# Kernel tuning notes

Measured on AMD Instinct MI355X. Metric: run time of the kernel, lower is better.

Reference implementation:

```python
import jax, jax.numpy as jnp
import numpy as np

K = 8192  # num_embeddings
D = 512   # embedding_dim
BETA = 0.25


def setup_inputs() -> dict:
    key = jax.random.key(0)
    k1, k2, k3 = jax.random.split(key, 3)
    B, T = 64, 512
    latents = jax.random.normal(k1, (B, T, D), dtype=jnp.float32)
    # nn.Embedding weight initialized uniform(-1/K, 1/K)
    emb = jax.random.uniform(k2, (K, D), dtype=jnp.float32, minval=-1.0 / K, maxval=1.0 / K)
    gold_encoding_inds = jax.random.randint(k3, (B * T, 1), 0, K, dtype=jnp.int64 if jax.config.jax_enable_x64 else jnp.int32)
    return {"gold_encoding_inds": gold_encoding_inds, "latents": latents, "epc": 1, "emb": emb}


def reference(gold_encoding_inds, latents, epc, emb):
    B, T, _ = latents.shape
    flat = latents.reshape(B * T, D)  # [N, D]
    # squared euclidean distance to every codebook entry: [N, K]
    dist = (jnp.sum(flat * flat, axis=1, keepdims=True)
            + jnp.sum(emb * emb, axis=1)
            - 2.0 * jnp.matmul(flat, emb.T))
    encoding_inds = jnp.argmin(dist, axis=1)[:, None]  # [N, 1]
    # one-hot @ emb  ==  gather rows of emb
    quantized = emb[encoding_inds[:, 0]].reshape(B, T, D)
    # per-position MSE over the feature dim
    commitment_loss = jnp.mean((jax.lax.stop_gradient(quantized) - latents) ** 2, axis=-1)
    embedding_loss = jnp.mean((quantized - jax.lax.stop_gradient(latents)) ** 2, axis=-1)
    vq_loss = embedding_loss + BETA * commitment_loss  # [B, T]
    # straight-through estimator
    quantized = latents + jax.lax.stop_gradient(quantized - latents)
    correct = jnp.sum(gold_encoding_inds == encoding_inds)
    total = jnp.asarray(gold_encoding_inds.shape[0], dtype=jnp.int32)
    return quantized, vq_loss, encoding_inds.T, (correct, total)
```

## Files before the change

### kernel.cpp

```cpp
#include <hip/hip_runtime.h>
#include <math.h>

#define N_ROWS 32768
#define KCB    8192
#define DIM    512
#define BETA   0.25f
#define MARGIN 2e-3f
#define FLAG_SLACK 1e-4f
#define CAND_CAP 256

typedef __attribute__((ext_vector_type(4))) float  f32x4;

__device__ __forceinline__ unsigned short f2h(float x) {
    _Float16 h = (_Float16)x;
    return *(unsigned short*)&h;
}
__device__ __forceinline__ float h2f(unsigned short u) {
    _Float16 h = *(_Float16*)&u;
    return (float)h;
}

#define SQ_BLOCKS ((N_ROWS + KCB) / 8)
__global__ __launch_bounds__(256) void pre_kernel(
        const float* __restrict__ lat, const float* __restrict__ emb,
        float* __restrict__ row_sq, float* __restrict__ emb_sq,
        unsigned char* __restrict__ latq, unsigned char* __restrict__ embq,
        int* __restrict__ counter) {
    if (blockIdx.x < SQ_BLOCKS) {
#pragma clang fp contract(off)
        if (blockIdx.x == 0 && threadIdx.x == 0) *counter = 0;
        const int w    = threadIdx.x >> 6;
        const int lane = threadIdx.x & 63;
        const int half = lane >> 5;
        const int L    = lane & 31;
        const int b    = L >> 3, j = L & 7;
        const int row  = blockIdx.x * 8 + w * 2 + half;
        const float* p = (row < N_ROWS) ? (lat + (size_t)row * DIM)
                                        : (emb + (size_t)(row - N_ROWS) * DIM);
        const float* q = p + 128 * b + j;
        float a0 = q[0];
        float r  = a0 * a0;
        for (int i = 1; i < 16; ++i) {
            float a = q[8 * i];
            float s = a * a;
            r = r + s;
        }
        r = r + __shfl_xor(r, 1);
        r = r + __shfl_xor(r, 2);
        r = r + __shfl_xor(r, 4);
        r = r + __shfl_xor(r, 8);
        r = r + __shfl_xor(r, 16);
        if (L == 0) {
            if (row < N_ROWS) row_sq[row] = r;
            else              emb_sq[row - N_ROWS] = r;
        }
    } else {
        const size_t NL8 = (size_t)N_ROWS * DIM / 8;
        const size_t NE8 = (size_t)KCB * DIM / 8;
        size_t g = (size_t)(blockIdx.x - SQ_BLOCKS) * 256 + threadIdx.x;
        const float* src; unsigned char* dst; size_t i; float sc;
        if (g < NL8)            { src = lat; dst = latq; i = g;       sc = 1.0f; }
        else if (g < NL8 + NE8) { src = emb; dst = embq; i = g - NL8; sc = 8192.0f; }
        else return;
        float4 v0 = ((const float4*)src)[2 * i];
        float4 v1 = ((const float4*)src)[2 * i + 1];
        int lo = __builtin_amdgcn_cvt_pk_fp8_f32(v0.x * sc, v0.y * sc, 0,  false);
        lo     = __builtin_amdgcn_cvt_pk_fp8_f32(v0.z * sc, v0.w * sc, lo, true);
        int hi = __builtin_amdgcn_cvt_pk_fp8_f32(v1.x * sc, v1.y * sc, 0,  false);
        hi     = __builtin_amdgcn_cvt_pk_fp8_f32(v1.z * sc, v1.w * sc, hi, true);
        ((int2*)dst)[i] = make_int2(lo, hi);
    }
}

__device__ __forceinline__ void load16_to_lds(const void* g, void* l) {
    __builtin_amdgcn_global_load_lds(
        (const __attribute__((address_space(1))) unsigned int*)g,
        (__attribute__((address_space(3))) unsigned int*)l, 16, 0, 0);
}

__global__ __launch_bounds__(256, 3) void gemm_kernel(
        const unsigned char* __restrict__ latq,
        const unsigned char* __restrict__ embq,
        const float* __restrict__ emb_sq,
        unsigned int* __restrict__ packed) {
    __shared__ unsigned char Ac[4 * 128 * 16];
    __shared__ unsigned char Br[4 * 128 * 16];

    const int tid   = threadIdx.x;
    const int w     = tid >> 6;
    const int lane  = tid & 63;
    const int q     = lane >> 4;
    const int m16   = lane & 15;
    const int row0  = blockIdx.x * 128;
    const int code0 = blockIdx.y * 128;
    const int wc    = 64 * (w >> 1);
    const int rbase = 64 * (w & 1);

    float sev[4][4];
#pragma unroll
    for (int r = 0; r < 4; ++r)
#pragma unroll
        for (int reg = 0; reg < 4; ++reg)
            sev[r][reg] = emb_sq[code0 + wc + 16 * r + 4 * q + reg];

    f32x4 acc[4][4];
#pragma unroll
    for (int r = 0; r < 4; ++r)
#pragma unroll
        for (int c = 0; c < 4; ++c) acc[r][c] = (f32x4){0.f, 0.f, 0.f, 0.f};

    for (int k0 = 0; k0 < DIM; k0 += 64) {
#pragma unroll
        for (int i = 0; i < 4; ++i) {
            int cid = w * 4 + i;
            if (cid < 8) {
                int p = cid >> 1, h = cid & 1;
                const unsigned char* g = embq +
                    (size_t)(code0 + h * 64 + lane) * DIM + k0 + p * 16;
                load16_to_lds(g, &Ac[(p * 128 + h * 64) * 16]);
            } else {
                int c2 = cid - 8, p = c2 >> 1, h = c2 & 1;
                const unsigned char* g = latq +
                    (size_t)(row0 + h * 64 + lane) * DIM + k0 + p * 16;
                load16_to_lds(g, &Br[(p * 128 + h * 64) * 16]);
            }
        }
        __syncthreads();
#pragma unroll
        for (int kk = 0; kk < 2; ++kk) {
            long a[4], b[4];
            const int p  = 2 * kk + (q >> 1);
            const int hf = (q & 1) * 8;
#pragma unroll
            for (int r = 0; r < 4; ++r)
                a[r] = *(const long*)&Ac[(p * 128 + wc + 16 * r + m16) * 16 + hf];
#pragma unroll
            for (int c = 0; c < 4; ++c)
                b[c] = *(const long*)&Br[(p * 128 + rbase + 16 * c + m16) * 16 + hf];
#pragma unroll
            for (int r = 0; r < 4; ++r)
#pragma unroll
                for (int c = 0; c < 4; ++c)
                    acc[r][c] = __builtin_amdgcn_mfma_f32_16x16x32_fp8_fp8(
                        a[r], b[c], acc[r][c], 0, 0, 0);
        }
        __syncthreads();
    }

    const float inv = 1.0f / 4096.0f;
#pragma unroll
    for (int c = 0; c < 4; ++c) {
        unsigned pk[4];
#pragma unroll
        for (int r = 0; r < 4; ++r) {
            float s0 = sev[r][0] - acc[r][c][0] * inv;
            float s1 = sev[r][1] - acc[r][c][1] * inv;
            float s2 = sev[r][2] - acc[r][c][2] * inv;
            float s3 = sev[r][3] - acc[r][c][3] * inv;
            float mn = fminf(fminf(s0, s1), fminf(s2, s3));
            mn = fminf(mn, __shfl_xor(mn, 16));
            mn = fminf(mn, __shfl_xor(mn, 32));
            float t = mn + MARGIN;
            unsigned nib = (s0 <= t ? 1u : 0u) | (s1 <= t ? 2u : 0u)
                         | (s2 <= t ? 4u : 0u) | (s3 <= t ? 8u : 0u);
            nib <<= (4 * q);
            nib |= (unsigned)__shfl_xor((int)nib, 16);
            nib |= (unsigned)__shfl_xor((int)nib, 32);
            pk[r] = ((unsigned)f2h(mn)) | (nib << 16);
        }
        if (lane < 16) {
            int grow = row0 + rbase + 16 * c + m16;
            int base = (code0 + wc) >> 4;
            *(uint4*)&packed[(size_t)grow * 512 + base] =
                make_uint4(pk[0], pk[1], pk[2], pk[3]);
        }
    }
}

__global__ __launch_bounds__(256) void argmin_out_kernel(
        const float* __restrict__ lat, const float* __restrict__ emb,
        const float* __restrict__ row_sq, const float* __restrict__ emb_sq,
        const unsigned int* __restrict__ packed,
        const int* __restrict__ gold,
        float* __restrict__ out, int* __restrict__ counter) {
    __shared__ float xs[4][DIM];
    __shared__ int   s_cnt[4];
    __shared__ int   s_list[4][CAND_CAP];
    const int w    = threadIdx.x >> 6;
    const int lane = threadIdx.x & 63;
    const int row  = blockIdx.x * 4 + w;

    {
        const float4* xp = (const float4*)(lat + (size_t)row * DIM);
        ((float4*)xs[w])[lane]      = xp[lane];
        ((float4*)xs[w])[lane + 64] = xp[lane + 64];
    }
    const float sx = row_sq[row];
    const float* xw = xs[w];

    unsigned u[8];
    {
        const uint4* tb = (const uint4*)(packed + (size_t)row * 512 + lane * 8);
        uint4 v0 = tb[0], v1 = tb[1];
        u[0] = v0.x; u[1] = v0.y; u[2] = v0.z; u[3] = v0.w;
        u[4] = v1.x; u[5] = v1.y; u[6] = v1.z; u[7] = v1.w;
    }
    float tm[8];
#pragma unroll
    for (int j = 0; j < 8; ++j) tm[j] = h2f((unsigned short)(u[j] & 0xFFFFu));
    float m = tm[0];
#pragma unroll
    for (int j = 1; j < 8; ++j) m = fminf(m, tm[j]);
#pragma unroll
    for (int off = 1; off < 64; off <<= 1)
        m = fminf(m, __shfl_xor(m, off));
    const float thresh = m + (MARGIN + FLAG_SLACK);

    if (lane == 0) s_cnt[w] = 0;
    __syncthreads();
#pragma unroll
    for (int j = 0; j < 8; ++j) {
        if (tm[j] <= thresh) {
            int g = lane * 8 + j;
            unsigned bm = u[j] >> 16;
            while (bm) {
                int b = __ffs(bm) - 1;
                bm &= bm - 1;
                int pos = atomicAdd(&s_cnt[w], 1);
                if (pos < CAND_CAP) s_list[w][pos] = g * 16 + b;
            }
        }
    }
    __syncthreads();
    const int cnt = min(s_cnt[w], CAND_CAP);

    float bd = INFINITY;
    int   bi = 0x7fffffff;
    for (int base = 0; base < cnt; base += 64) {
        int ci = base + lane;
        float dvl = INFINITY;
        int   cl  = 0x7fffffff;
        if (ci < cnt) {
            int code = s_list[w][ci];
            const float* ep = emb + (size_t)code * DIM;
            float acc = 0.0f;
            for (int d = 0; d < DIM; d += 8) {
                float ev[8], xv[8];
#pragma unroll
                for (int t = 0; t < 8; ++t) { ev[t] = ep[d + t]; xv[t] = xw[d + t]; }
#pragma unroll
                for (int t = 0; t < 8; ++t) acc = fmaf(xv[t], ev[t], acc);
            }
            float a = sx + emb_sq[code];
            dvl = a - 2.0f * acc;
            cl  = code;
        }
        if (dvl < bd || (dvl == bd && cl < bi)) { bd = dvl; bi = cl; }
    }
#pragma unroll
    for (int off = 1; off < 64; off <<= 1) {
        float od = __shfl_xor(bd, off);
        int   oi = __shfl_xor(bi, off);
        if (od < bd || (od == bd && oi < bi)) { bd = od; bi = oi; }
    }
    const int idx = bi;

    const float4* e4 = (const float4*)(emb + (size_t)idx * DIM);
    float4*       q4 = (float4*)(out + (size_t)row * DIM);
    q4[lane]      = e4[lane];
    q4[lane + 64] = e4[lane + 64];

    float r = 0.0f;
    if (lane < 32) {
        const int b = lane >> 3, j = lane & 7;
        const float* ep = emb + (size_t)idx * DIM + b * 128 + j;
        const float* xp = xw + b * 128 + j;
        for (int i = 0; i < 16; ++i) {
            float dq = ep[8 * i] - xp[8 * i];
            float s  = dq * dq;
            r = (i == 0) ? s : (r + s);
        }
    }
    for (int mm = 1; mm <= 16; mm <<= 1) {
        float o = __shfl_xor(r, mm);
        r = r + o;
    }
    if (lane == 0) {
        float mean = r * (1.0f / 512.0f);
        float v    = mean + 0.25f * mean;
        out[(size_t)N_ROWS * DIM + row]          = v;
        out[(size_t)N_ROWS * DIM + N_ROWS + row] = (float)idx;
        if (gold[row] == idx) atomicAdd(counter, 1);
    }
}

__global__ void tail_kernel(const int* __restrict__ counter,
                            float* __restrict__ out) {
    if (threadIdx.x == 0 && blockIdx.x == 0) {
        const size_t off = (size_t)N_ROWS * DIM + 2 * (size_t)N_ROWS;
        out[off]     = (float)(*counter);
        out[off + 1] = (float)N_ROWS;
    }
}

__global__ __launch_bounds__(256) void sq_kernel(
        const float* __restrict__ lat, const float* __restrict__ emb,
        float* __restrict__ row_sq, float* __restrict__ emb_sq) {
#pragma clang fp contract(off)
    const int w    = threadIdx.x >> 6;
    const int lane = threadIdx.x & 63;
    const int half = lane >> 5;
    const int L    = lane & 31;
    const int b    = L >> 3, j = L & 7;
    const int row  = blockIdx.x * 8 + w * 2 + half;
    if (row >= N_ROWS + KCB) return;
    const float* p = (row < N_ROWS) ? (lat + (size_t)row * DIM)
                                    : (emb + (size_t)(row - N_ROWS) * DIM);
    const float* q = p + 128 * b + j;
    float a0 = q[0];
    float r  = a0 * a0;
    for (int i = 1; i < 16; ++i) {
        float a = q[8 * i];
        float s = a * a;
        r = r + s;
    }
    r = r + __shfl_xor(r, 1);
    r = r + __shfl_xor(r, 2);
    r = r + __shfl_xor(r, 4);
    r = r + __shfl_xor(r, 8);
    r = r + __shfl_xor(r, 16);
    if (L == 0) {
        if (row < N_ROWS) row_sq[row] = r;
        else              emb_sq[row - N_ROWS] = r;
    }
}

#define BM 64
#define BK 128
#define BD 32
__global__ __launch_bounds__(256) void dist_kernel(
        const float* __restrict__ lat, const float* __restrict__ emb,
        const float* __restrict__ row_sq, const float* __restrict__ emb_sq,
        int* __restrict__ enc) {
    __shared__ float xsh[BD][BM];
    __shared__ float esh[BD][BK];
    const int tid  = threadIdx.x;
    const int trow = tid >> 4;
    const int tcol = tid & 15;
    const int row0 = blockIdx.x * BM;
    float bd[4]; int bi[4];
    for (int i = 0; i < 4; ++i) { bd[i] = INFINITY; bi[i] = 0; }
    float sx[4];
    for (int i = 0; i < 4; ++i) sx[i] = row_sq[row0 + 4 * trow + i];
    for (int kt = 0; kt < KCB; kt += BK) {
        float acc[4][8] = {};
        for (int d0 = 0; d0 < DIM; d0 += BD) {
            for (int f = tid; f < BM * BD / 4; f += 256) {
                int r = f >> 3, c4 = f & 7;
                float4 v = *(const float4*)(lat + (size_t)(row0 + r) * DIM + d0 + 4 * c4);
                xsh[4 * c4 + 0][r] = v.x; xsh[4 * c4 + 1][r] = v.y;
                xsh[4 * c4 + 2][r] = v.z; xsh[4 * c4 + 3][r] = v.w;
            }
            for (int f = tid; f < BK * BD / 4; f += 256) {
                int r = f >> 3, c4 = f & 7;
                float4 v = *(const float4*)(emb + (size_t)(kt + r) * DIM + d0 + 4 * c4);
                esh[4 * c4 + 0][r] = v.x; esh[4 * c4 + 1][r] = v.y;
                esh[4 * c4 + 2][r] = v.z; esh[4 * c4 + 3][r] = v.w;
            }
            __syncthreads();
            for (int dd = 0; dd < BD; ++dd) {
                float4 xv  = *(const float4*)&xsh[dd][4 * trow];
                float4 ev0 = *(const float4*)&esh[dd][8 * tcol];
                float4 ev1 = *(const float4*)&esh[dd][8 * tcol + 4];
                float xr[4] = { xv.x, xv.y, xv.z, xv.w };
                float ec[8] = { ev0.x, ev0.y, ev0.z, ev0.w, ev1.x, ev1.y, ev1.z, ev1.w };
                for (int r = 0; r < 4; ++r)
                    for (int c = 0; c < 8; ++c)
                        acc[r][c] = fmaf(xr[r], ec[c], acc[r][c]);
            }
            __syncthreads();
        }
        for (int c = 0; c < 8; ++c) {
            int   code = kt + 8 * tcol + c;
            float se   = emb_sq[code];
            for (int r = 0; r < 4; ++r) {
                float a  = sx[r] + se;
                float dv = a - 2.0f * acc[r][c];
                if (dv < bd[r]) { bd[r] = dv; bi[r] = code; }
            }
        }
    }
    for (int off = 1; off < 16; off <<= 1) {
        for (int r = 0; r < 4; ++r) {
            float od = __shfl_xor(bd[r], off);
            int   oi = __shfl_xor(bi[r], off);
            if (od < bd[r] || (od == bd[r] && oi < bi[r])) { bd[r] = od; bi[r] = oi; }
        }
    }
    if (tcol == 0)
        for (int r = 0; r < 4; ++r)
            enc[row0 + 4 * trow + r] = bi[r];
}

__global__ void out_kernel(const float* __restrict__ lat,
                           const float* __restrict__ emb,
                           const int* __restrict__ gold,
                           const int* __restrict__ enc,
                           float* __restrict__ out,
                           int* __restrict__ counter) {
#pragma clang fp contract(off)
    const int gid  = blockIdx.x * blockDim.x + threadIdx.x;
    const int row  = gid >> 6;
    const int lane = threadIdx.x & 63;
    if (row >= N_ROWS) return;
    const int idx = enc[row];
    const float4* e4 = (const float4*)(emb + (size_t)idx * DIM);
    float4*       q4 = (float4*)(out + (size_t)row * DIM);
    q4[lane]      = e4[lane];
    q4[lane + 64] = e4[lane + 64];
    float r = 0.0f;
    if (lane < 32) {
        const int b = lane >> 3, j = lane & 7;
        const float* ep = emb + (size_t)idx * DIM + b * 128 + j;
        const float* xp = lat + (size_t)row * DIM + b * 128 + j;
        for (int i = 0; i < 16; ++i) {
            float dq = ep[8 * i] - xp[8 * i];
            float s  = dq * dq;
            r = (i == 0) ? s : (r + s);
        }
    }
    for (int m = 1; m <= 16; m <<= 1) {
        float o = __shfl_xor(r, m);
        r = r + o;
    }
    if (lane == 0) {
        float mean = r * (1.0f / 512.0f);
        float v    = mean + 0.25f * mean;
        out[(size_t)N_ROWS * DIM + row]          = v;
        out[(size_t)N_ROWS * DIM + N_ROWS + row] = (float)idx;
        if (gold[row] == idx) atomicAdd(counter, 1);
    }
}

extern "C" void kernel_launch(void* const* d_in, const int* in_sizes, int n_in,
                              void* d_out, int out_size, void* d_ws, size_t ws_size,
                              hipStream_t stream) {
    (void)in_sizes; (void)n_in; (void)out_size;
    const int*   gold = (const int*)d_in[0];
    const float* lat  = (const float*)d_in[1];
    const float* emb  = (const float*)d_in[3];
    float* out = (float*)d_out;

    const size_t SZ_LATQ = (size_t)N_ROWS * DIM;
    const size_t SZ_EMBQ = (size_t)KCB * DIM;
    const size_t SZ_PK   = (size_t)N_ROWS * 512 * 4;
    const size_t SZ_SMALL = (size_t)N_ROWS * 4 + (size_t)KCB * 4 + 256;
    const size_t NEEDED = SZ_LATQ + SZ_EMBQ + SZ_PK + SZ_SMALL;

    if (ws_size >= NEEDED) {
        unsigned char* w8 = (unsigned char*)d_ws;
        unsigned char* latq    = w8;
        unsigned char* embq    = w8 + SZ_LATQ;
        unsigned int*  packed  = (unsigned int*)(w8 + SZ_LATQ + SZ_EMBQ);
        float*         row_sq  = (float*)(w8 + SZ_LATQ + SZ_EMBQ + SZ_PK);
        float*         emb_sq  = row_sq + N_ROWS;
        int*           counter = (int*)(emb_sq + KCB);

        const int pre_blocks = SQ_BLOCKS + (N_ROWS + KCB) * (DIM / 8) / 256;
        pre_kernel<<<pre_blocks, 256, 0, stream>>>(
            lat, emb, row_sq, emb_sq, latq, embq, counter);
        dim3 ggrid(N_ROWS / 128, KCB / 128);
        gemm_kernel<<<ggrid, 256, 0, stream>>>(latq, embq, emb_sq, packed);
        argmin_out_kernel<<<N_ROWS / 4, 256, 0, stream>>>(
            lat, emb, row_sq, emb_sq, packed, gold, out, counter);
        tail_kernel<<<1, 64, 0, stream>>>(counter, out);
    } else {
        float* row_sq  = (float*)d_ws;
        float* emb_sq  = row_sq + N_ROWS;
        int*   enc     = (int*)(emb_sq + KCB);
        int*   counter = enc + N_ROWS;
        hipMemsetAsync(counter, 0, sizeof(int), stream);
        sq_kernel<<<(N_ROWS + KCB) / 8, 256, 0, stream>>>(lat, emb, row_sq, emb_sq);
        dist_kernel<<<N_ROWS / BM, 256, 0, stream>>>(lat, emb, row_sq, emb_sq, enc);
        out_kernel<<<N_ROWS / 4, 256, 0, stream>>>(lat, emb, gold, enc, out, counter);
        tail_kernel<<<1, 64, 0, stream>>>(counter, out);
    }
}
```

Baseline: 648.6 us.

## Use scaled 16x16x128 FP8 MFMA with swizzled 128-wide LDS tiles

Replaces the 16x16x32 FP8 MFMA inner loop with the gfx950 scaled MFMA 16x16x128 f8f6f4 instruction, using unit scales. The K tile grows from 64 to 128 bytes per stage, so there are half as many barrier pairs. The LDS layout changes to row-major 128-byte rows with an XOR swizzle so the 16-byte lane reads avoid bank conflicts. The larger tiles use 32KB of LDS per block and more registers, which could reduce occupancy under launch_bounds(256,3). The swizzle indexing also has to match the layout exactly to stay correct.

```diff
diff --git a/kernel.cpp b/kernel.cpp
--- a/kernel.cpp
+++ b/kernel.cpp
@@ -10,6 +10,8 @@
 #define CAND_CAP 256
 
 typedef __attribute__((ext_vector_type(4))) float  f32x4;
+typedef __attribute__((ext_vector_type(4))) int    i32x4;
+typedef __attribute__((ext_vector_type(8))) int    i32x8;
 
 __device__ __forceinline__ unsigned short f2h(float x) {
     _Float16 h = (_Float16)x;
@@ -83,8 +85,8 @@
         const unsigned char* __restrict__ embq,
         const float* __restrict__ emb_sq,
         unsigned int* __restrict__ packed) {
-    __shared__ unsigned char Ac[4 * 128 * 16];
-    __shared__ unsigned char Br[4 * 128 * 16];
+    __shared__ unsigned char Ac[128 * 128];
+    __shared__ unsigned char Br[128 * 128];
 
     const int tid   = threadIdx.x;
     const int w     = tid >> 6;
@@ -96,56 +98,67 @@
     const int wc    = 64 * (w >> 1);
     const int rbase = 64 * (w & 1);
 
+    int soff[8];
+#pragma unroll
+    for (int i = 0; i < 8; ++i) {
+        int cid   = w * 8 + i;
+        int h     = cid & 15;
+        int base0 = (cid < 16) ? code0 : row0;
+        soff[i] = (base0 + h * 8 + (lane >> 3)) * DIM
+                + (((lane & 7) ^ (lane >> 3)) << 4);
+    }
+
+    f32x4 acc[4][4];
+#pragma unroll
+    for (int r = 0; r < 4; ++r)
+#pragma unroll
+        for (int c = 0; c < 4; ++c) acc[r][c] = (f32x4){0.f, 0.f, 0.f, 0.f};
+
+    const int sw = (m16 & 7) << 4;
+
+    for (int k0 = 0; k0 < DIM; k0 += 128) {
+#pragma unroll
+        for (int i = 0; i < 8; ++i) {
+            int cid = w * 8 + i;
+            const unsigned char* g = ((cid < 16) ? embq : latq) + soff[i] + k0;
+            unsigned char* l = ((cid < 16) ? Ac : Br) + (cid & 15) * 1024;
+            load16_to_lds(g, l);
+        }
+        __syncthreads();
+
+        i32x8 af[4];
+#pragma unroll
+        for (int r = 0; r < 4; ++r) {
+            int roff = (wc + 16 * r + m16) * 128;
+            i32x4 lo = *(const i32x4*)&Ac[roff + ((q * 32) ^ sw)];
+            i32x4 hi = *(const i32x4*)&Ac[roff + ((q * 32 + 16) ^ sw)];
+            af[r] = (i32x8){lo[0], lo[1], lo[2], lo[3],
+                            hi[0], hi[1], hi[2], hi[3]};
+        }
+#pragma unroll
+        for (int c = 0; c < 4; ++c) {
+            int roff = (rbase + 16 * c + m16) * 128;
+            i32x4 lo = *(const i32x4*)&Br[roff + ((q * 32) ^ sw)];
+            i32x4 hi = *(const i32x4*)&Br[roff + ((q * 32 + 16) ^ sw)];
+            i32x8 bv = (i32x8){lo[0], lo[1], lo[2], lo[3],
+                               hi[0], hi[1], hi[2], hi[3]};
+#pragma unroll
+            for (int r = 0; r < 4; ++r)
+                acc[r][c] = __builtin_amdgcn_mfma_scale_f32_16x16x128_f8f6f4(
+                    af[r], bv, acc[r][c],
+                    0, 0,
+                    0, 0x7F7F7F7F,
+                    0, 0x7F7F7F7F);
+        }
+        __syncthreads();
+    }
+
     float sev[4][4];
 #pragma unroll
     for (int r = 0; r < 4; ++r)
 #pragma unroll
         for (int reg = 0; reg < 4; ++reg)
             sev[r][reg] = emb_sq[code0 + wc + 16 * r + 4 * q + reg];
-
-    f32x4 acc[4][4];
-#pragma unroll
-    for (int r = 0; r < 4; ++r)
-#pragma unroll
-        for (int c = 0; c < 4; ++c) acc[r][c] = (f32x4){0.f, 0.f, 0.f, 0.f};
-
-    for (int k0 = 0; k0 < DIM; k0 += 64) {
-#pragma unroll
-        for (int i = 0; i < 4; ++i) {
-            int cid = w * 4 + i;
-            if (cid < 8) {
-                int p = cid >> 1, h = cid & 1;
-                const unsigned char* g = embq +
-                    (size_t)(code0 + h * 64 + lane) * DIM + k0 + p * 16;
-                load16_to_lds(g, &Ac[(p * 128 + h * 64) * 16]);
-            } else {
-                int c2 = cid - 8, p = c2 >> 1, h = c2 & 1;
-                const unsigned char* g = latq +
-                    (size_t)(row0 + h * 64 + lane) * DIM + k0 + p * 16;
-                load16_to_lds(g, &Br[(p * 128 + h * 64) * 16]);
-            }
-        }
-        __syncthreads();
-#pragma unroll
-        for (int kk = 0; kk < 2; ++kk) {
-            long a[4], b[4];
-            const int p  = 2 * kk + (q >> 1);
-            const int hf = (q & 1) * 8;
-#pragma unroll
-            for (int r = 0; r < 4; ++r)
-                a[r] = *(const long*)&Ac[(p * 128 + wc + 16 * r + m16) * 16 + hf];
-#pragma unroll
-            for (int c = 0; c < 4; ++c)
-                b[c] = *(const long*)&Br[(p * 128 + rbase + 16 * c + m16) * 16 + hf];
-#pragma unroll
-            for (int r = 0; r < 4; ++r)
-#pragma unroll
-                for (int c = 0; c < 4; ++c)
-                    acc[r][c] = __builtin_amdgcn_mfma_f32_16x16x32_fp8_fp8(
-                        a[r], b[c], acc[r][c], 0, 0, 0);
-        }
-        __syncthreads();
-    }
 
     const float inv = 1.0f / 4096.0f;
 #pragma unroll
```

After: 580.9 us. -10.4%, faster.
